# Optimization experiments

Hardware: AMD Instinct MI355X
Metric: run time of the kernel (lower is better)

The kernel has to match this reference:

```python
import jax, jax.numpy as jnp
import numpy as np

E = 256      # emb_size
H = 100      # ff_sim hidden
B, TQ, TK = 16, 128, 128


def setup_inputs() -> dict:
    key = jax.random.key(0)
    ks = jax.random.split(key, 8)
    queries = jax.random.normal(ks[0], (B, TQ, E), dtype=jnp.float32)
    keys = jax.random.normal(ks[1], (B, TK, E), dtype=jnp.float32)
    query_masks = jnp.ones((B, TQ), dtype=jnp.float32)
    key_masks = jnp.ones((B, TK), dtype=jnp.float32)
    # xavier_uniform bounds: sqrt(6/(fan_in+fan_out))
    def xavier(k, shape):
        fan_out, fan_in = shape
        lim = np.sqrt(6.0 / (fan_in + fan_out))
        return jax.random.uniform(k, shape, jnp.float32, -lim, lim)
    W1 = xavier(ks[2], (H, 2 * E))          # linear_ff_sim[0].weight
    b1 = jnp.zeros((H,), dtype=jnp.float32)  # linear_ff_sim[0].bias
    W2 = xavier(ks[3], (1, H))              # linear_ff_sim[2].weight (no bias)
    Wlast = xavier(ks[4], (E, 2 * E))       # linear_last.weight
    blast = jnp.zeros((E,), dtype=jnp.float32)
    return {"queries": queries, "keys": keys, "query_masks": query_masks,
            "key_masks": key_masks, "W1": W1, "b1": b1, "W2": W2,
            "Wlast": Wlast, "blast": blast}


def reference(queries, keys, query_masks, key_masks, W1, b1, W2, Wlast, blast):
    # forward calls attention_fc(keys, queries, key_masks, query_masks):
    #   attn queries = keys,  attn keys = queries,
    #   attn query_masks = key_masks, attn key_masks = query_masks.
    e = queries.shape[-1]
    # Additive-attention MLP score, decomposed: cat([keys_i, queries_j]) @ W1^T
    #   = keys_i @ W1[:, :E]^T + queries_j @ W1[:, E:]^T
    a = jnp.einsum('bie,he->bih', keys, W1[:, :e])      # [B,Tk,H]
    c = jnp.einsum('bje,he->bjh', queries, W1[:, e:])   # [B,Tq,H]
    h = jnp.tanh(a[:, :, None, :] + c[:, None, :, :] + b1)  # [B,Tk,Tq,H]
    sim = jnp.einsum('bijh,h->bij', h, W2[0])           # [B,Tk,Tq]
    neg = jnp.asarray(-2.0 ** 32 + 1, sim.dtype)
    sim = jnp.where(query_masks[:, None, :] == 0, neg, sim)
    sim = jax.nn.softmax(sim, axis=-1)
    sim = sim * key_masks[:, :, None]
    keys_attn = jnp.einsum('bij,bje->bie', sim, queries)  # [B,Tk,E]
    feature_mul = keys_attn * keys
    d = keys_attn - keys
    feature_sub = d * d
    feature_last = jnp.concatenate([feature_mul, feature_sub], axis=-1)  # [B,Tk,2E]
    return jax.nn.relu(jnp.einsum('bif,ef->bie', feature_last, Wlast) + blast)
```

## Files before the change

### kernel.cpp

```cpp
#include <hip/hip_runtime.h>


namespace {
constexpr int B  = 16;
constexpr int TQ = 128;
constexpr int TK = 128;
constexpr int E  = 256;
constexpr int H  = 100;
constexpr int HP = 112;
constexpr int G  = 4;
}

typedef __attribute__((ext_vector_type(8))) short short8;
typedef __attribute__((ext_vector_type(4))) float f32x4;

__device__ __forceinline__ unsigned short f2bf(float f) {
  unsigned u = __builtin_bit_cast(unsigned, f);
  u = (u + 0x7FFFu + ((u >> 16) & 1u)) >> 16;
  return (unsigned short)u;
}

__global__ __launch_bounds__(256) void prep_ac(
    const float* __restrict__ queries, const float* __restrict__ keys,
    const float* __restrict__ W1, const float* __restrict__ b1,
    const float* __restrict__ Wlast,
    float* __restrict__ A, float* __restrict__ C,
    unsigned short* __restrict__ Wb ) {
  constexpr int RPB = 16;
  __shared__ float xs[RPB * E];
  const int t  = threadIdx.x;
  const int r0 = blockIdx.x * RPB;
  const bool isA = (r0 < B * TK);
  const float* src = isA ? (keys + (size_t)r0 * E)
                         : (queries + (size_t)(r0 - B * TK) * E);
  float* dst = isA ? (A + (size_t)r0 * HP)
                   : (C + (size_t)(r0 - B * TK) * HP);

  {
    const int base = blockIdx.x * 512 + t * 2;
    float2 w = *(const float2*)(Wlast + base);
    Wb[base]     = f2bf(w.x);
    Wb[base + 1] = f2bf(w.y);
  }

  {
    const float4* s4 = (const float4*)src;
    float4* x4 = (float4*)xs;
    #pragma unroll
    for (int m = 0; m < RPB * E / 4 / 256; ++m)
      x4[t + m * 256] = s4[t + m * 256];
  }
  __syncthreads();

  const int h0 = (t & 63) * 2;
  const int rg = t >> 6;
  if (h0 < H) {
    float acc0[4], acc1[4];
    const float bi0 = isA ? b1[h0] : 0.0f;
    const float bi1 = isA ? b1[h0 + 1] : 0.0f;
    #pragma unroll
    for (int i = 0; i < 4; ++i) { acc0[i] = bi0; acc1[i] = bi1; }
    const float4* w40 = (const float4*)(W1 + (size_t)h0 * (2 * E) + (isA ? 0 : E));
    const float4* w41 = (const float4*)(W1 + (size_t)(h0 + 1) * (2 * E) + (isA ? 0 : E));
    const float4* x4  = (const float4*)xs + (size_t)rg * 4 * (E / 4);
    #pragma unroll 4
    for (int e4 = 0; e4 < E / 4; ++e4) {
      float4 wa = w40[e4], wb = w41[e4];
      #pragma unroll
      for (int i = 0; i < 4; ++i) {
        float4 xv = x4[i * (E / 4) + e4];
        acc0[i] += wa.x * xv.x + wa.y * xv.y + wa.z * xv.z + wa.w * xv.w;
        acc1[i] += wb.x * xv.x + wb.y * xv.y + wb.z * xv.z + wb.w * xv.w;
      }
    }
    #pragma unroll
    for (int i = 0; i < 4; ++i)
      *(float2*)(dst + (size_t)(rg * 4 + i) * HP + h0) = make_float2(acc0[i], acc1[i]);
  } else if (h0 < HP) {
    #pragma unroll
    for (int i = 0; i < 4; ++i)
      *(float2*)(dst + (size_t)(rg * 4 + i) * HP + h0) = make_float2(0.0f, 0.0f);
  }
}

__global__ __launch_bounds__(512) void attn_core(
    const float* __restrict__ queries, const float* __restrict__ keys,
    const float* __restrict__ qmask, const float* __restrict__ kmask,
    const float* __restrict__ W2, const float* __restrict__ A,
    const float* __restrict__ C, unsigned short* __restrict__ feat ) {
  __shared__ float a_s[G * HP];
  __shared__ float w2s[HP];
  __shared__ float qm[TQ];
  __shared__ float simP[G * 512];
  __shared__ float pL[G * TQ];
  __shared__ float red[8];

  const int t   = threadIdx.x;
  const int blk = blockIdx.x;
  const int b   = blk >> 5;
  const int i0  = (blk & 31) * G;

  if (t < G * HP / 4)
    ((float4*)a_s)[t] = ((const float4*)(A + ((size_t)b * TK + i0) * HP))[t];
  if (t < HP) w2s[t] = (t < H) ? W2[t] : 0.0f;
  if (t < TQ) qm[t]  = qmask[b * TQ + t];
  __syncthreads();

  const int j = t & (TQ - 1);
  const int q = t >> 7;
  float4 cr[7], wr[7];
  float wsum = 0.0f;
  {
    const float4* c4 = (const float4*)(C + ((size_t)b * TQ + j) * HP + q * 28);
    const float4* w4 = (const float4*)w2s + q * 7;
    #pragma unroll
    for (int k = 0; k < 7; ++k) {
      cr[k] = c4[k];
      wr[k] = w4[k];
      wsum += wr[k].x + wr[k].y + wr[k].z + wr[k].w;
    }
  }
  {
    const float4* a4p = (const float4*)a_s + q * 7;
    #pragma unroll
    for (int g = 0; g < G; ++g) {
      float s = 0.0f;
      #pragma unroll
      for (int k = 0; k < 7; ++k) {
        float4 a4 = a4p[g * (HP / 4) + k];
        float x0 = a4.x + cr[k].x, x1 = a4.y + cr[k].y;
        float x2 = a4.z + cr[k].z, x3 = a4.w + cr[k].w;
        s = fmaf(wr[k].x, __builtin_amdgcn_rcpf(__expf(x0 + x0) + 1.0f), s);
        s = fmaf(wr[k].y, __builtin_amdgcn_rcpf(__expf(x1 + x1) + 1.0f), s);
        s = fmaf(wr[k].z, __builtin_amdgcn_rcpf(__expf(x2 + x2) + 1.0f), s);
        s = fmaf(wr[k].w, __builtin_amdgcn_rcpf(__expf(x3 + x3) + 1.0f), s);
      }
      simP[g * 512 + t] = wsum - 2.0f * s;
    }
  }
  __syncthreads();

  {
    const int g2 = t >> 7, j2 = t & 127;
    const float* sp = simP + g2 * 512 + j2;
    float sv = sp[0] + sp[128] + sp[256] + sp[384];
    if (qm[j2] == 0.0f) sv = -4294967295.0f;
    float p = __expf(sv);
    float s = p;
    #pragma unroll
    for (int off = 1; off < 64; off <<= 1) s += __shfl_xor(s, off, 64);
    if ((t & 63) == 0) red[t >> 6] = s;
    __syncthreads();
    pL[t] = p / (red[g2 * 2] + red[g2 * 2 + 1]);
  }
  __syncthreads();

  {
    const int e = t & 255, gh = t >> 8;
    float ka0 = 0.0f, ka1 = 0.0f;
    const float* qb = queries + (size_t)b * TQ * E + e;
    const float4* p4 = (const float4*)pL;
    for (int j4 = 0; j4 < TQ / 4; ++j4) {
      float4 p0 = p4[(gh * 2) * 32 + j4];
      float4 p1 = p4[(gh * 2 + 1) * 32 + j4];
      #pragma unroll
      for (int c = 0; c < 4; ++c) {
        float qv = qb[(size_t)(j4 * 4 + c) * E];
        ka0 = fmaf(((const float*)&p0)[c], qv, ka0);
        ka1 = fmaf(((const float*)&p1)[c], qv, ka1);
      }
    }
    #pragma unroll
    for (int gg = 0; gg < 2; ++gg) {
      const int g = gh * 2 + gg;
      const float ka = gg ? ka1 : ka0;
      const float kmv = kmask[b * TK + i0 + g];
      const float kav = ka * kmv;
      const float kv  = keys[((size_t)b * TK + i0 + g) * E + e];
      const size_t row = (size_t)(b * TK + i0 + g) * (2 * E);
      feat[row + e]     = f2bf(kav * kv);
      float d = kav - kv;
      feat[row + E + e] = f2bf(d * d);
    }
  }
}

__global__ __launch_bounds__(256) void last_gemm(
    const unsigned short* __restrict__ Wb ,
    const float* __restrict__ blast, float* __restrict__ out) {
  __shared__ short A_s[16 * 520];
  __shared__ short B_s[256 * 72];
  const int t  = threadIdx.x;
  const int m0 = blockIdx.x * 16;

  {
    const uint4* src = (const uint4*)out;
    #pragma unroll
    for (int i = 0; i < 4; ++i) {
      int idx = t + i * 256;
      int r = idx >> 6, c = idx & 63;
      *(uint4*)(A_s + r * 520 + c * 8) = src[(size_t)(m0 + r) * 64 + c];
    }
  }
  __syncthreads();

  f32x4 acc[4];
  #pragma unroll
  for (int nt = 0; nt < 4; ++nt) acc[nt] = f32x4{0.f, 0.f, 0.f, 0.f};

  const int wave = t >> 6, lane = t & 63;
  const int nsub = wave * 64;
  const int m    = lane & 15, kq = lane >> 4;

  for (int kc = 0; kc < 8; ++kc) {
    #pragma unroll
    for (int i = 0; i < 8; ++i) {
      int idx = t + i * 256;
      int r = idx >> 3, p = idx & 7;
      *(uint4*)(B_s + r * 72 + p * 8) =
          ((const uint4*)(Wb + (size_t)r * 512 + kc * 64))[p];
    }
    __syncthreads();
    #pragma unroll
    for (int ks = 0; ks < 2; ++ks) {
      short8 a = *(const short8*)(A_s + m * 520 + kc * 64 + ks * 32 + kq * 8);
      #pragma unroll
      for (int nt = 0; nt < 4; ++nt) {
        short8 bf = *(const short8*)(B_s + (nsub + nt * 16 + m) * 72 + ks * 32 + kq * 8);
        acc[nt] = __builtin_amdgcn_mfma_f32_16x16x32_bf16(a, bf, acc[nt], 0, 0, 0);
      }
    }
    __syncthreads();
  }

  const int col = lane & 15;
  const int rbase = m0 + (lane >> 4) * 4;
  #pragma unroll
  for (int nt = 0; nt < 4; ++nt) {
    const int e = nsub + nt * 16 + col;
    const float bl = blast[e];
    #pragma unroll
    for (int r = 0; r < 4; ++r)
      out[(size_t)(rbase + r) * 256 + e] = fmaxf(acc[nt][r] + bl, 0.0f);
  }
}

extern "C" void kernel_launch(void* const* d_in, const int* in_sizes, int n_in,
                              void* d_out, int out_size, void* d_ws, size_t ws_size,
                              hipStream_t stream) {
  (void)in_sizes; (void)n_in; (void)out_size; (void)ws_size;
  const float* queries = (const float*)d_in[0];
  const float* keys    = (const float*)d_in[1];
  const float* qmask   = (const float*)d_in[2];
  const float* kmask   = (const float*)d_in[3];
  const float* W1      = (const float*)d_in[4];
  const float* b1      = (const float*)d_in[5];
  const float* W2      = (const float*)d_in[6];
  const float* Wlast   = (const float*)d_in[7];
  const float* blast   = (const float*)d_in[8];
  float* out = (float*)d_out;

  float* A = (float*)d_ws;
  float* C = A + (size_t)B * TK * HP;
  unsigned short* Wb = (unsigned short*)(C + (size_t)B * TQ * HP);

  prep_ac<<<dim3(256), dim3(256), 0, stream>>>(queries, keys, W1, b1, Wlast, A, C, Wb);
  attn_core<<<dim3(B * (TK / G)), dim3(512), 0, stream>>>(
      queries, keys, qmask, kmask, W2, A, C, (unsigned short*)out);
  last_gemm<<<dim3(B * TK / 16), dim3(256), 0, stream>>>(Wb, blast, out);
}
```

Measured before the change: 109.0 us.

## Compute W1 projections with bf16 MFMA after a separate conversion pass

```diff
diff --git a/kernel.cpp b/kernel.cpp
--- a/kernel.cpp
+++ b/kernel.cpp
@@ -20,66 +20,93 @@
   return (unsigned short)u;
 }
 
-__global__ __launch_bounds__(256) void prep_ac(
+__global__ __launch_bounds__(256) void convert_bf16(
     const float* __restrict__ queries, const float* __restrict__ keys,
-    const float* __restrict__ W1, const float* __restrict__ b1,
-    const float* __restrict__ Wlast,
-    float* __restrict__ A, float* __restrict__ C,
-    unsigned short* __restrict__ Wb ) {
-  constexpr int RPB = 16;
-  __shared__ float xs[RPB * E];
+    const float* __restrict__ W1, const float* __restrict__ Wlast,
+    unsigned short* __restrict__ Xb, unsigned short* __restrict__ Wb1,
+    unsigned short* __restrict__ Wb) {
+  const int blk = blockIdx.x, t = threadIdx.x;
+  if (blk < 1024) {
+    const int idx = blk * 1024 + t * 4;
+    const int row = idx >> 8, e = idx & 255;
+    const float* src = (row < B * TK) ? keys + (size_t)row * E + e
+                                      : queries + (size_t)(row - B * TK) * E + e;
+    float4 v = *(const float4*)src;
+    ushort4 o = make_ushort4(f2bf(v.x), f2bf(v.y), f2bf(v.z), f2bf(v.w));
+    *(ushort4*)(Xb + idx) = o;
+  } else if (blk < 1080) {
+    const int idx = (blk - 1024) * 1024 + t * 4;
+    const int h = idx >> 9;
+    float4 v = (h < H) ? *(const float4*)(W1 + idx)
+                       : make_float4(0.f, 0.f, 0.f, 0.f);
+    ushort4 o = make_ushort4(f2bf(v.x), f2bf(v.y), f2bf(v.z), f2bf(v.w));
+    *(ushort4*)(Wb1 + idx) = o;
+  } else {
+    const int idx = (blk - 1080) * 1024 + t * 4;
+    float4 v = *(const float4*)(Wlast + idx);
+    ushort4 o = make_ushort4(f2bf(v.x), f2bf(v.y), f2bf(v.z), f2bf(v.w));
+    *(ushort4*)(Wb + idx) = o;
+  }
+}
+
+__global__ __launch_bounds__(256) void prep_mfma(
+    const unsigned short* __restrict__ Xb, const unsigned short* __restrict__ Wb1,
+    const float* __restrict__ b1, float* __restrict__ A, float* __restrict__ C) {
+  __shared__ short Bs[112 * 264];
+  __shared__ short As[16 * 264];
   const int t  = threadIdx.x;
-  const int r0 = blockIdx.x * RPB;
-  const bool isA = (r0 < B * TK);
-  const float* src = isA ? (keys + (size_t)r0 * E)
-                         : (queries + (size_t)(r0 - B * TK) * E);
-  float* dst = isA ? (A + (size_t)r0 * HP)
-                   : (C + (size_t)(r0 - B * TK) * HP);
-
-  {
-    const int base = blockIdx.x * 512 + t * 2;
-    float2 w = *(const float2*)(Wlast + base);
-    Wb[base]     = f2bf(w.x);
-    Wb[base + 1] = f2bf(w.y);
-  }
-
-  {
-    const float4* s4 = (const float4*)src;
-    float4* x4 = (float4*)xs;
-    #pragma unroll
-    for (int m = 0; m < RPB * E / 4 / 256; ++m)
-      x4[t + m * 256] = s4[t + m * 256];
-  }
-  __syncthreads();
-
-  const int h0 = (t & 63) * 2;
-  const int rg = t >> 6;
-  if (h0 < H) {
-    float acc0[4], acc1[4];
-    const float bi0 = isA ? b1[h0] : 0.0f;
-    const float bi1 = isA ? b1[h0 + 1] : 0.0f;
-    #pragma unroll
-    for (int i = 0; i < 4; ++i) { acc0[i] = bi0; acc1[i] = bi1; }
-    const float4* w40 = (const float4*)(W1 + (size_t)h0 * (2 * E) + (isA ? 0 : E));
-    const float4* w41 = (const float4*)(W1 + (size_t)(h0 + 1) * (2 * E) + (isA ? 0 : E));
-    const float4* x4  = (const float4*)xs + (size_t)rg * 4 * (E / 4);
-    #pragma unroll 4
-    for (int e4 = 0; e4 < E / 4; ++e4) {
-      float4 wa = w40[e4], wb = w41[e4];
-      #pragma unroll
-      for (int i = 0; i < 4; ++i) {
-        float4 xv = x4[i * (E / 4) + e4];
-        acc0[i] += wa.x * xv.x + wa.y * xv.y + wa.z * xv.z + wa.w * xv.w;
-        acc1[i] += wb.x * xv.x + wb.y * xv.y + wb.z * xv.z + wb.w * xv.w;
-      }
-    }
-    #pragma unroll
-    for (int i = 0; i < 4; ++i)
-      *(float2*)(dst + (size_t)(rg * 4 + i) * HP + h0) = make_float2(acc0[i], acc1[i]);
-  } else if (h0 < HP) {
-    #pragma unroll
-    for (int i = 0; i < 4; ++i)
-      *(float2*)(dst + (size_t)(rg * 4 + i) * HP + h0) = make_float2(0.0f, 0.0f);
+  const int m0 = blockIdx.x * 16;
+  const bool isA = (m0 < B * TK);
+  const int koff = isA ? 0 : 256;
+  float* dst = isA ? (A + (size_t)m0 * HP)
+                   : (C + (size_t)(m0 - B * TK) * HP);
+
+  #pragma unroll
+  for (int i = 0; i < 14; ++i) {
+    const int idx = i * 256 + t;
+    const int h = idx >> 5, seg = idx & 31;
+    *(uint4*)(Bs + h * 264 + seg * 8) =
+        *(const uint4*)(Wb1 + (size_t)h * 512 + koff + seg * 8);
+  }
+  #pragma unroll
+  for (int i = 0; i < 2; ++i) {
+    const int idx = i * 256 + t;
+    const int r = idx >> 5, seg = idx & 31;
+    *(uint4*)(As + r * 264 + seg * 8) =
+        *(const uint4*)(Xb + (size_t)(m0 + r) * 256 + seg * 8);
+  }
+  __syncthreads();
+
+  const int wave = t >> 6, lane = t & 63;
+  const int m = lane & 15, kq = lane >> 4;
+  const int nt0 = wave, nt1 = wave + 4;
+  f32x4 acc0 = {0.f, 0.f, 0.f, 0.f}, acc1 = {0.f, 0.f, 0.f, 0.f};
+
+  #pragma unroll
+  for (int kc = 0; kc < 8; ++kc) {
+    short8 a = *(const short8*)(As + m * 264 + kc * 32 + kq * 8);
+    short8 bv0 = *(const short8*)(Bs + (nt0 * 16 + m) * 264 + kc * 32 + kq * 8);
+    acc0 = __builtin_amdgcn_mfma_f32_16x16x32_bf16(a, bv0, acc0, 0, 0, 0);
+    if (nt1 < 7) {
+      short8 bv1 = *(const short8*)(Bs + (nt1 * 16 + m) * 264 + kc * 32 + kq * 8);
+      acc1 = __builtin_amdgcn_mfma_f32_16x16x32_bf16(a, bv1, acc1, 0, 0, 0);
+    }
+  }
+
+  const int rbase = (lane >> 4) * 4;
+  {
+    const int h = nt0 * 16 + m;
+    const float bias = (isA && h < H) ? b1[h] : 0.0f;
+    #pragma unroll
+    for (int r = 0; r < 4; ++r)
+      dst[(size_t)(rbase + r) * HP + h] = acc0[r] + bias;
+  }
+  if (nt1 < 7) {
+    const int h = nt1 * 16 + m;
+    const float bias = (isA && h < H) ? b1[h] : 0.0f;
+    #pragma unroll
+    for (int r = 0; r < 4; ++r)
+      dst[(size_t)(rbase + r) * HP + h] = acc1[r] + bias;
   }
 }
 
@@ -262,9 +289,13 @@
 
   float* A = (float*)d_ws;
   float* C = A + (size_t)B * TK * HP;
-  unsigned short* Wb = (unsigned short*)(C + (size_t)B * TQ * HP);
-
-  prep_ac<<<dim3(256), dim3(256), 0, stream>>>(queries, keys, W1, b1, Wlast, A, C, Wb);
+  unsigned short* Wb  = (unsigned short*)(C + (size_t)B * TQ * HP);
+  unsigned short* Wb1 = Wb + (size_t)256 * 512;
+  unsigned short* Xb  = Wb1 + (size_t)112 * 512;
+
+  convert_bf16<<<dim3(1208), dim3(256), 0, stream>>>(
+      queries, keys, W1, Wlast, Xb, Wb1, Wb);
+  prep_mfma<<<dim3(256), dim3(256), 0, stream>>>(Xb, Wb1, b1, A, C);
   attn_core<<<dim3(B * (TK / G)), dim3(512), 0, stream>>>(
       queries, keys, qmask, kmask, W2, A, C, (unsigned short*)out);
   last_gemm<<<dim3(B * TK / 16), dim3(256), 0, stream>>>(Wb, blast, out);
```

Result: faster. 99.08 us (-9.1%).
